# Optimization experiments

Hardware: AMD Instinct MI355X
Metric: run time of the kernel (lower is better)

Reference implementation:

```python
import jax, jax.numpy as jnp
import numpy as np

SCALE = 1.0

def _sq_dist(p0, p1):
    # p0: [B,N,3], p1: [B,M,3] -> [B,N,M] squared euclidean distances
    n0 = jnp.sum(p0 * p0, axis=-1)  # [B,N]
    n1 = jnp.sum(p1 * p1, axis=-1)  # [B,M]
    inner = jnp.einsum('bnd,bmd->bnm', p0, p1)  # [B,N,M]
    return n0[:, :, None] + n1[:, None, :] - 2.0 * inner

def setup_inputs() -> dict:
    key = jax.random.key(0)
    k0, k1 = jax.random.split(key)
    template = jax.random.normal(k0, (4, 8192, 3), dtype=jnp.float32)
    source = jax.random.normal(k1, (4, 8192, 3), dtype=jnp.float32)
    return {"template": template, "source": source}

def reference(template, source):
    p0 = template / SCALE
    p1 = source / SCALE
    d = _sq_dist(p0, p1)  # [B,N,M]
    # nearest neighbor in each direction, averaged over points
    d01 = jnp.mean(jnp.min(d, axis=2), axis=1)  # template -> source, [B]
    d10 = jnp.mean(jnp.min(d, axis=1), axis=1)  # source -> template, [B]
    return d01 + d10  # per-batch chamfer distance (reduction='none')
```

## Files before the change

### kernel.cpp

```cpp
#include <hip/hip_runtime.h>
#include <stdint.h>


typedef __bf16 bf16x8 __attribute__((ext_vector_type(8)));
typedef float  f32x16 __attribute__((ext_vector_type(16)));
typedef float  f32x4  __attribute__((ext_vector_type(4)));

constexpr int B     = 4;
constexpr int NPTS  = 8192;
constexpr int BLOCK = 256;
constexpr int QPB   = 256;
constexpr int QBLKS = NPTS / QPB;
constexpr int CH    = 4;
constexpr int CPTS  = NPTS / CH;
constexpr int SPTS  = 512;
constexpr int NPASS = CPTS / SPTS;
constexpr int TPP   = SPTS / 32;
constexpr int GRPS  = NPTS / 32;
constexpr int PASSBYTES = SPTS * 32;
constexpr int RSTRIDE = 36;
constexpr int SMEMB = BLOCK * RSTRIDE * 4;
constexpr size_t CMBYTES = (size_t)2 * B * CH * NPTS * sizeof(float);

__device__ inline void gload_lds16(const void* g, void* l) {
    __builtin_amdgcn_global_load_lds(
        (const __attribute__((address_space(1))) uint32_t*)g,
        (__attribute__((address_space(3))) uint32_t*)l, 16, 0, 0);
}

__global__ __launch_bounds__(BLOCK) void chamfer_prep(
    const float* __restrict__ tpl, const float* __restrict__ src,
    bf16x8* __restrict__ efrag)
{
    const int pt  = blockIdx.x * BLOCK + threadIdx.x;
    const int c   = blockIdx.y;
    const int b   = c & (B - 1);
    const int dir = c >> 2;
    const float* db = (dir == 0 ? src : tpl) + (size_t)b * NPTS * 3;

    float x = db[3 * pt], y = db[3 * pt + 1], z = db[3 * pt + 2];
    float n = -0.5f * (x * x + y * y + z * z);
    __bf16 hx = (__bf16)x, hy = (__bf16)y, hz = (__bf16)z;
    __bf16 lx = (__bf16)(x - (float)hx);
    __bf16 ly = (__bf16)(y - (float)hy);
    __bf16 lz = (__bf16)(z - (float)hz);
    __bf16 nh = (__bf16)n;
    __bf16 nl = (__bf16)(n - (float)nh);
    const __bf16 zb = (__bf16)0.0f;

    const int gi = pt >> 5, sl = pt & 31;
    size_t gb = ((size_t)c * GRPS + gi) * 64;
    efrag[gb + sl]      = (bf16x8){hx, hy, hz, lx, ly, lz, hx, hy};
    efrag[gb + 32 + sl] = (bf16x8){hz, nh, nl, lx, ly, lz, zb, zb};
}

__global__ __launch_bounds__(BLOCK, 4) void chamfer_sweep(
    const float* __restrict__ tpl, const float* __restrict__ src,
    const bf16x8* __restrict__ efrag,
    float* __restrict__ cm)
{
    __shared__ char smem[SMEMB];
    const int tid = threadIdx.x;
    const int l   = tid & 63;
    const int w   = tid >> 6;
    const int h   = l >> 5;
    const int r32 = l & 31;
    const int c   = blockIdx.z;
    const int b   = c & (B - 1);
    const int dir = c >> 2;
    const float* q = (dir == 0 ? tpl : src) + (size_t)b * NPTS * 3;
    const char* eb = (const char*)efrag
                   + ((size_t)c * GRPS + blockIdx.y * (CPTS / 32)) * 1024;

    #pragma unroll
    for (int i = 0; i < 4; ++i) {
        int off = (w * 4 + i) * 1024;
        gload_lds16(eb + off + l * 16, smem + off);
    }

    float* qs = (float*)(smem + 32768);
    {
        const float4* qg4 = (const float4*)(q + (size_t)blockIdx.x * QPB * 3);
        if (tid < 192) ((float4*)qs)[tid] = qg4[tid];
    }
    __syncthreads();

    const __bf16 one = (__bf16)1.0f, zb = (__bf16)0.0f;
    bf16x8 fa[2];
    #pragma unroll
    for (int f = 0; f < 2; ++f) {
        int qloc = w * 64 + f * 32 + r32;
        float x = qs[3 * qloc], y = qs[3 * qloc + 1], z = qs[3 * qloc + 2];
        __bf16 hx = (__bf16)x, hy = (__bf16)y, hz = (__bf16)z;
        __bf16 lx = (__bf16)(x - (float)hx);
        __bf16 ly = (__bf16)(y - (float)hy);
        __bf16 lz = (__bf16)(z - (float)hz);
        if (h == 0) fa[f] = (bf16x8){hx, hy, hz, hx, hy, hz, lx, ly};
        else        fa[f] = (bf16x8){lz, one, one, lx, ly, lz, zb, zb};
    }

    f32x16 best0, best1, zc;
    #pragma unroll
    for (int r = 0; r < 16; ++r) { best0[r] = -3.4e38f; best1[r] = -3.4e38f; zc[r] = 0.0f; }

    const int idx0 = h * 32 + r32;
    for (int gp = 0; gp < NPASS; ++gp) {
        __syncthreads();
        if (gp + 1 < NPASS) {
            const char* ebn = eb + (gp + 1) * PASSBYTES;
            char* dst = smem + ((gp + 1) & 1) * 16384;
            #pragma unroll
            for (int i = 0; i < 4; ++i) {
                int off = (w * 4 + i) * 1024;
                gload_lds16(ebn + off + l * 16, dst + off);
            }
        }
        const bf16x8* sb = (const bf16x8*)(smem + (gp & 1) * 16384);
        __builtin_amdgcn_s_setprio(1);
        #pragma unroll
        for (int t = 0; t < TPP; t += 2) {
            bf16x8 bv0 = sb[t * 64 + idx0];
            bf16x8 bv1 = sb[(t + 1) * 64 + idx0];
            f32x16 d0 = __builtin_amdgcn_mfma_f32_32x32x16_bf16(fa[0], bv0, zc, 0, 0, 0);
            f32x16 d1 = __builtin_amdgcn_mfma_f32_32x32x16_bf16(fa[0], bv1, zc, 0, 0, 0);
            f32x16 e0 = __builtin_amdgcn_mfma_f32_32x32x16_bf16(fa[1], bv0, zc, 0, 0, 0);
            f32x16 e1 = __builtin_amdgcn_mfma_f32_32x32x16_bf16(fa[1], bv1, zc, 0, 0, 0);
            #pragma unroll
            for (int r = 0; r < 16; ++r)
                best0[r] = fmaxf(fmaxf(best0[r], d0[r]), d1[r]);
            #pragma unroll
            for (int r = 0; r < 16; ++r)
                best1[r] = fmaxf(fmaxf(best1[r], e0[r]), e1[r]);
        }
        __builtin_amdgcn_s_setprio(0);
    }

    __syncthreads();
    float* red = (float*)smem;
    #pragma unroll
    for (int r = 0; r < 16; ++r) {
        int row = (r & 3) + 8 * (r >> 2) + 4 * h;
        red[(w * 64 + row) * RSTRIDE + r32]      = best0[r];
        red[(w * 64 + 32 + row) * RSTRIDE + r32] = best1[r];
    }
    __syncthreads();
    const float* rr = red + tid * RSTRIDE;
    float m = -3.4e38f;
    #pragma unroll
    for (int j = 0; j < 8; ++j) {
        f32x4 v = *(const f32x4*)(rr + 4 * j);
        m = fmaxf(m, fmaxf(fmaxf(v.x, v.y), fmaxf(v.z, v.w)));
    }
    cm[((size_t)c * CH + blockIdx.y) * NPTS + blockIdx.x * QPB + tid] = m;
}

__global__ __launch_bounds__(256) void chamfer_final(
    const float* __restrict__ tpl, const float* __restrict__ src,
    const float* __restrict__ cm, float* __restrict__ out)
{
    __shared__ float red[256];
    const int b = blockIdx.x;
    const float* q0 = tpl + (size_t)b * NPTS * 3;
    const float* q1 = src + (size_t)b * NPTS * 3;
    const float* c0 = cm + (size_t)b * CH * NPTS;
    const float* c1 = cm + (size_t)(B + b) * CH * NPTS;

    float s = 0.f;
    for (int i = threadIdx.x; i < NPTS; i += 256) {
        float m0 = fmaxf(fmaxf(c0[i], c0[NPTS + i]),
                         fmaxf(c0[2 * NPTS + i], c0[3 * NPTS + i]));
        float x = q0[3 * i], y = q0[3 * i + 1], z = q0[3 * i + 2];
        s += fmaf(m0, -2.0f, x * x + y * y + z * z);
        float m1 = fmaxf(fmaxf(c1[i], c1[NPTS + i]),
                         fmaxf(c1[2 * NPTS + i], c1[3 * NPTS + i]));
        x = q1[3 * i]; y = q1[3 * i + 1]; z = q1[3 * i + 2];
        s += fmaf(m1, -2.0f, x * x + y * y + z * z);
    }
    red[threadIdx.x] = s;
    __syncthreads();
    #pragma unroll
    for (int off = 128; off > 0; off >>= 1) {
        if (threadIdx.x < off) red[threadIdx.x] += red[threadIdx.x + off];
        __syncthreads();
    }
    if (threadIdx.x == 0) out[b] = red[0] * (1.0f / NPTS);
}

extern "C" void kernel_launch(void* const* d_in, const int* in_sizes, int n_in,
                              void* d_out, int out_size, void* d_ws, size_t ws_size,
                              hipStream_t stream) {
    const float* tpl = (const float*)d_in[0];
    const float* src = (const float*)d_in[1];
    float* out = (float*)d_out;
    float* cm      = (float*)d_ws;
    bf16x8* efrag  = (bf16x8*)((char*)d_ws + CMBYTES);

    chamfer_prep <<<dim3(NPTS / BLOCK, 2 * B), BLOCK, 0, stream>>>(tpl, src, efrag);
    chamfer_sweep<<<dim3(QBLKS, CH, 2 * B),    BLOCK, 0, stream>>>(tpl, src, efrag, cm);
    chamfer_final<<<B, 256, 0, stream>>>(tpl, src, cm, out);
}
```

Baseline: 40.67 us.

## Fuse final reduction into sweep via last-block atomic counter

Removes the separate final reduction kernel. Each sweep block atomically increments a per-batch counter after writing its partial minima, and the last block for that batch performs the mean reduction. The counter is reset in the prep kernel. Query points are now loaded straight from global memory instead of staged through shared memory, which drops one barrier, and the occupancy hint in launch bounds changes from 4 to 3. This saves one kernel launch but adds atomics and fences, and the final reduction becomes a serial tail in one block per batch.

```diff
diff --git a/kernel.cpp b/kernel.cpp
--- a/kernel.cpp
+++ b/kernel.cpp
@@ -20,7 +20,9 @@
 constexpr int PASSBYTES = SPTS * 32;
 constexpr int RSTRIDE = 36;
 constexpr int SMEMB = BLOCK * RSTRIDE * 4;
+constexpr int BLKS_PER_B = 2 * CH * QBLKS;
 constexpr size_t CMBYTES = (size_t)2 * B * CH * NPTS * sizeof(float);
+constexpr size_t EFBYTES = (size_t)2 * B * NPTS * 32;
 
 __device__ inline void gload_lds16(const void* g, void* l) {
     __builtin_amdgcn_global_load_lds(
@@ -30,13 +32,15 @@
 
 __global__ __launch_bounds__(BLOCK) void chamfer_prep(
     const float* __restrict__ tpl, const float* __restrict__ src,
-    bf16x8* __restrict__ efrag)
+    bf16x8* __restrict__ efrag, unsigned* __restrict__ cnt)
 {
     const int pt  = blockIdx.x * BLOCK + threadIdx.x;
     const int c   = blockIdx.y;
     const int b   = c & (B - 1);
     const int dir = c >> 2;
     const float* db = (dir == 0 ? src : tpl) + (size_t)b * NPTS * 3;
+
+    if (blockIdx.x == 0 && c == 0 && threadIdx.x < B) cnt[threadIdx.x] = 0u;
 
     float x = db[3 * pt], y = db[3 * pt + 1], z = db[3 * pt + 2];
     float n = -0.5f * (x * x + y * y + z * z);
@@ -54,12 +58,16 @@
     efrag[gb + 32 + sl] = (bf16x8){hz, nh, nl, lx, ly, lz, zb, zb};
 }
 
-__global__ __launch_bounds__(BLOCK, 4) void chamfer_sweep(
+__global__ __launch_bounds__(BLOCK, 3) void chamfer_sweep(
     const float* __restrict__ tpl, const float* __restrict__ src,
     const bf16x8* __restrict__ efrag,
-    float* __restrict__ cm)
+    float* __restrict__ cm,
+    unsigned* __restrict__ cnt,
+    float* __restrict__ out)
 {
     __shared__ char smem[SMEMB];
+    __shared__ unsigned lastflag;
+
     const int tid = threadIdx.x;
     const int l   = tid & 63;
     const int w   = tid >> 6;
@@ -69,6 +77,7 @@
     const int b   = c & (B - 1);
     const int dir = c >> 2;
     const float* q = (dir == 0 ? tpl : src) + (size_t)b * NPTS * 3;
+    const int qbase = blockIdx.x * QPB + w * 64;
     const char* eb = (const char*)efrag
                    + ((size_t)c * GRPS + blockIdx.y * (CPTS / 32)) * 1024;
 
@@ -78,19 +87,12 @@
         gload_lds16(eb + off + l * 16, smem + off);
     }
 
-    float* qs = (float*)(smem + 32768);
-    {
-        const float4* qg4 = (const float4*)(q + (size_t)blockIdx.x * QPB * 3);
-        if (tid < 192) ((float4*)qs)[tid] = qg4[tid];
-    }
-    __syncthreads();
-
     const __bf16 one = (__bf16)1.0f, zb = (__bf16)0.0f;
     bf16x8 fa[2];
     #pragma unroll
     for (int f = 0; f < 2; ++f) {
-        int qloc = w * 64 + f * 32 + r32;
-        float x = qs[3 * qloc], y = qs[3 * qloc + 1], z = qs[3 * qloc + 2];
+        int qi = qbase + f * 32 + r32;
+        float x = q[3 * qi], y = q[3 * qi + 1], z = q[3 * qi + 2];
         __bf16 hx = (__bf16)x, hy = (__bf16)y, hz = (__bf16)z;
         __bf16 lx = (__bf16)(x - (float)hx);
         __bf16 ly = (__bf16)(y - (float)hy);
@@ -151,39 +153,49 @@
         f32x4 v = *(const f32x4*)(rr + 4 * j);
         m = fmaxf(m, fmaxf(fmaxf(v.x, v.y), fmaxf(v.z, v.w)));
     }
-    cm[((size_t)c * CH + blockIdx.y) * NPTS + blockIdx.x * QPB + tid] = m;
-}
-
-__global__ __launch_bounds__(256) void chamfer_final(
-    const float* __restrict__ tpl, const float* __restrict__ src,
-    const float* __restrict__ cm, float* __restrict__ out)
-{
-    __shared__ float red[256];
-    const int b = blockIdx.x;
-    const float* q0 = tpl + (size_t)b * NPTS * 3;
-    const float* q1 = src + (size_t)b * NPTS * 3;
-    const float* c0 = cm + (size_t)b * CH * NPTS;
-    const float* c1 = cm + (size_t)(B + b) * CH * NPTS;
-
-    float s = 0.f;
-    for (int i = threadIdx.x; i < NPTS; i += 256) {
-        float m0 = fmaxf(fmaxf(c0[i], c0[NPTS + i]),
-                         fmaxf(c0[2 * NPTS + i], c0[3 * NPTS + i]));
-        float x = q0[3 * i], y = q0[3 * i + 1], z = q0[3 * i + 2];
-        s += fmaf(m0, -2.0f, x * x + y * y + z * z);
-        float m1 = fmaxf(fmaxf(c1[i], c1[NPTS + i]),
-                         fmaxf(c1[2 * NPTS + i], c1[3 * NPTS + i]));
-        x = q1[3 * i]; y = q1[3 * i + 1]; z = q1[3 * i + 2];
-        s += fmaf(m1, -2.0f, x * x + y * y + z * z);
-    }
-    red[threadIdx.x] = s;
+    __hip_atomic_store(
+        &cm[((size_t)c * CH + blockIdx.y) * NPTS + blockIdx.x * QPB + tid], m,
+        __ATOMIC_RELAXED, __HIP_MEMORY_SCOPE_AGENT);
+
+    __threadfence();
+    if (tid == 0) {
+        unsigned old = atomicAdd(&cnt[b], 1u);
+        lastflag = (old == (unsigned)(BLKS_PER_B - 1)) ? 1u : 0u;
+    }
     __syncthreads();
-    #pragma unroll
-    for (int off = 128; off > 0; off >>= 1) {
-        if (threadIdx.x < off) red[threadIdx.x] += red[threadIdx.x + off];
+    if (lastflag) {
+        const float* q0 = tpl + (size_t)b * NPTS * 3;
+        const float* q1 = src + (size_t)b * NPTS * 3;
+        const float* c0 = cm + (size_t)b * CH * NPTS;
+        const float* c1 = cm + (size_t)(B + b) * CH * NPTS;
+        float s = 0.f;
+        for (int i = tid; i < NPTS; i += 256) {
+            float a0 = __hip_atomic_load(&c0[i],            __ATOMIC_RELAXED, __HIP_MEMORY_SCOPE_AGENT);
+            float a1 = __hip_atomic_load(&c0[NPTS + i],     __ATOMIC_RELAXED, __HIP_MEMORY_SCOPE_AGENT);
+            float a2 = __hip_atomic_load(&c0[2 * NPTS + i], __ATOMIC_RELAXED, __HIP_MEMORY_SCOPE_AGENT);
+            float a3 = __hip_atomic_load(&c0[3 * NPTS + i], __ATOMIC_RELAXED, __HIP_MEMORY_SCOPE_AGENT);
+            float m0 = fmaxf(fmaxf(a0, a1), fmaxf(a2, a3));
+            float x = q0[3 * i], y = q0[3 * i + 1], z = q0[3 * i + 2];
+            s += fmaf(m0, -2.0f, x * x + y * y + z * z);
+            a0 = __hip_atomic_load(&c1[i],            __ATOMIC_RELAXED, __HIP_MEMORY_SCOPE_AGENT);
+            a1 = __hip_atomic_load(&c1[NPTS + i],     __ATOMIC_RELAXED, __HIP_MEMORY_SCOPE_AGENT);
+            a2 = __hip_atomic_load(&c1[2 * NPTS + i], __ATOMIC_RELAXED, __HIP_MEMORY_SCOPE_AGENT);
+            a3 = __hip_atomic_load(&c1[3 * NPTS + i], __ATOMIC_RELAXED, __HIP_MEMORY_SCOPE_AGENT);
+            float m1 = fmaxf(fmaxf(a0, a1), fmaxf(a2, a3));
+            x = q1[3 * i]; y = q1[3 * i + 1]; z = q1[3 * i + 2];
+            s += fmaf(m1, -2.0f, x * x + y * y + z * z);
+        }
         __syncthreads();
-    }
-    if (threadIdx.x == 0) out[b] = red[0] * (1.0f / NPTS);
+        float* red2 = (float*)smem;
+        red2[tid] = s;
+        __syncthreads();
+        #pragma unroll
+        for (int off = 128; off > 0; off >>= 1) {
+            if (tid < off) red2[tid] += red2[tid + off];
+            __syncthreads();
+        }
+        if (tid == 0) out[b] = red2[0] * (1.0f / NPTS);
+    }
 }
 
 extern "C" void kernel_launch(void* const* d_in, const int* in_sizes, int n_in,
@@ -194,8 +206,8 @@
     float* out = (float*)d_out;
     float* cm      = (float*)d_ws;
     bf16x8* efrag  = (bf16x8*)((char*)d_ws + CMBYTES);
-
-    chamfer_prep <<<dim3(NPTS / BLOCK, 2 * B), BLOCK, 0, stream>>>(tpl, src, efrag);
-    chamfer_sweep<<<dim3(QBLKS, CH, 2 * B),    BLOCK, 0, stream>>>(tpl, src, efrag, cm);
-    chamfer_final<<<B, 256, 0, stream>>>(tpl, src, cm, out);
-}
+    unsigned* cnt  = (unsigned*)((char*)d_ws + CMBYTES + EFBYTES);
+
+    chamfer_prep <<<dim3(NPTS / BLOCK, 2 * B), BLOCK, 0, stream>>>(tpl, src, efrag, cnt);
+    chamfer_sweep<<<dim3(QBLKS, CH, 2 * B),    BLOCK, 0, stream>>>(tpl, src, efrag, cm, cnt, out);
+}
```

Result: slower. 99.07 us (+143.6%).
